# Performance work log

Measured on AMD Instinct MI355X. Metric: run time of the kernel, lower is better.

The kernel has to match this reference:

```python
import jax, jax.numpy as jnp
import numpy as np

EMB_DIM = 1024
NUM_HEADS = 16
HEAD_DIM = EMB_DIM // NUM_HEADS
B, S_Q, S_KV = 4, 2048, 2048


def setup_inputs() -> dict:
    key = jax.random.key(0)
    ks = jax.random.split(key, 12)
    s = EMB_DIM ** -0.5  # torch Linear default init scale (approx, uniform-like)
    inp = {
        "q": jax.random.normal(ks[0], (B, S_Q, EMB_DIM), jnp.float32),
        "k": jax.random.normal(ks[1], (B, S_KV, EMB_DIM), jnp.float32),
        "v": jax.random.normal(ks[2], (B, S_KV, EMB_DIM), jnp.float32),
        "mask": jax.random.randint(ks[3], (B, S_KV), 0, 2, jnp.int32),
        "Wq": jax.random.normal(ks[4], (EMB_DIM, EMB_DIM), jnp.float32) * s,
        "bq": jnp.zeros((EMB_DIM,), jnp.float32),
        "Wk": jax.random.normal(ks[5], (EMB_DIM, EMB_DIM), jnp.float32) * s,
        "bk": jnp.zeros((EMB_DIM,), jnp.float32),
        "Wv": jax.random.normal(ks[6], (EMB_DIM, EMB_DIM), jnp.float32) * s,
        "bv": jnp.zeros((EMB_DIM,), jnp.float32),
        "Wo": jax.random.normal(ks[7], (EMB_DIM, EMB_DIM), jnp.float32) * s,
        "bo": jnp.zeros((EMB_DIM,), jnp.float32),
    }
    return inp


def reference(q, k, v, mask, Wq, bq, Wk, bk, Wv, bv, Wo, bo):
    Bsz, Sq, E = q.shape
    Skv = k.shape[1]
    H, D = NUM_HEADS, HEAD_DIM
    scale = D ** -0.5

    # projections (torch Linear: x @ W.T + b)
    qh = (q @ Wq.T + bq).reshape(Bsz, Sq, H, D).transpose(0, 2, 1, 3)   # [B,H,Sq,D]
    kh = (k @ Wk.T + bk).reshape(Bsz, Skv, H, D).transpose(0, 2, 1, 3)  # [B,H,Skv,D]
    vh = (v @ Wv.T + bv).reshape(Bsz, Skv, H, D).transpose(0, 2, 1, 3)  # [B,H,Skv,D]

    attn = jnp.einsum("bhqd,bhkd->bhqk", qh, kh) * scale  # [B,H,Sq,Skv]

    valid = mask != 0                                      # [B,Skv]
    all_invalid = ~jnp.any(valid, axis=-1, keepdims=True)  # [B,1]
    safe = valid | all_invalid                             # reopened rows
    attn = jnp.where(safe[:, None, None, :], attn, -jnp.inf)

    attn = jax.nn.softmax(attn, axis=-1)
    attn = jnp.where(all_invalid.reshape(Bsz, 1, 1, 1), 0.0, attn)

    out = jnp.einsum("bhqk,bhkd->bhqd", attn, vh)          # [B,H,Sq,D]
    out = out.transpose(0, 2, 1, 3).reshape(Bsz, Sq, E)
    return out @ Wo.T + bo
```

## Files before the change

### kernel.cpp

```cpp
#include <hip/hip_runtime.h>
#include <hip/hip_bf16.h>

typedef short bh8 __attribute__((ext_vector_type(8)));
typedef float f32x4 __attribute__((ext_vector_type(4)));
typedef float f32x16 __attribute__((ext_vector_type(16)));
typedef float f2 __attribute__((ext_vector_type(2)));
typedef unsigned int uint4v __attribute__((ext_vector_type(4)));

#define GLOBAL_P(p) ((const __attribute__((address_space(1))) void*)(p))
#define LDS_P(p)    ((__attribute__((address_space(3))) void*)(p))

__device__ inline bh8 pack8(const float4& a, const float4& b) {
    union { bh8 v; __hip_bfloat16 h[8]; } u;
    u.h[0] = __float2bfloat16(a.x); u.h[1] = __float2bfloat16(a.y);
    u.h[2] = __float2bfloat16(a.z); u.h[3] = __float2bfloat16(a.w);
    u.h[4] = __float2bfloat16(b.x); u.h[5] = __float2bfloat16(b.y);
    u.h[6] = __float2bfloat16(b.z); u.h[7] = __float2bfloat16(b.w);
    return u.v;
}

__global__ __launch_bounds__(256) void cvt3(
    const float* __restrict__ a, const float* __restrict__ b, const float* __restrict__ c,
    __hip_bfloat16* __restrict__ oa, __hip_bfloat16* __restrict__ ob, __hip_bfloat16* __restrict__ oc)
{
    size_t i = ((size_t)blockIdx.x * 256 + threadIdx.x) * 8;
    float4 x0 = *(const float4*)(a + i), x1 = *(const float4*)(a + i + 4);
    *(bh8*)(oa + i) = pack8(x0, x1);
    float4 y0 = *(const float4*)(b + i), y1 = *(const float4*)(b + i + 4);
    *(bh8*)(ob + i) = pack8(y0, y1);
    float4 z0 = *(const float4*)(c + i), z1 = *(const float4*)(c + i + 4);
    *(bh8*)(oc + i) = pack8(z0, z1);
}

__global__ __launch_bounds__(256) void cvtW(
    const float* __restrict__ a, const float* __restrict__ b,
    const float* __restrict__ c, const float* __restrict__ d,
    __hip_bfloat16* __restrict__ o)
{
    int seg = blockIdx.x >> 9;
    const float* src = (seg == 0) ? a : (seg == 1) ? b : (seg == 2) ? c : d;
    size_t i = ((size_t)(blockIdx.x & 511) * 256 + threadIdx.x) * 8;
    float4 x0 = *(const float4*)(src + i), x1 = *(const float4*)(src + i + 4);
    *(bh8*)(o + (size_t)seg * 1048576 + i) = pack8(x0, x1);
}

template <typename TC>
__global__ __launch_bounds__(256) void gemm_bt(
    const __hip_bfloat16* __restrict__ A, const __hip_bfloat16* __restrict__ W,
    const float* __restrict__ bias, TC* __restrict__ C,
    int M, int N, int Ksz, float oscale)
{
    __shared__ __hip_bfloat16 As[128 * 64];
    __shared__ __hip_bfloat16 Bs[128 * 64];
    const int tid = threadIdx.x;
    const int l = tid & 63, w = tid >> 6;
    const int g4 = l >> 4, rl = l & 15;
    const int nb = N >> 7;
    const int bm = blockIdx.x / nb, bn = blockIdx.x % nb;
    const long m0 = (long)bm * 128, n0 = (long)bn * 128;

    const __hip_bfloat16* ag[4];
    const __hip_bfloat16* wg[4];
    int ldsbase[4];
#pragma unroll
    for (int i = 0; i < 4; ++i) {
        int c = i * 256 + tid;
        int row = c >> 3, c8 = c & 7;
        ag[i] = A + (m0 + row) * Ksz + c8 * 8;
        wg[i] = W + (n0 + row) * Ksz + c8 * 8;
        ldsbase[i] = (i * 256 + w * 64) * 8;
    }

    const int wr = w >> 1, wc = w & 1;
    f32x4 acc[4][4];
#pragma unroll
    for (int i = 0; i < 4; ++i)
#pragma unroll
        for (int j = 0; j < 4; ++j) acc[i][j] = f32x4{0.f, 0.f, 0.f, 0.f};

    const int nk = Ksz >> 6;
    for (int t = 0; t < nk; ++t) {
        __syncthreads();
#pragma unroll
        for (int i = 0; i < 4; ++i) {
            __builtin_amdgcn_global_load_lds(GLOBAL_P(ag[i]), LDS_P((__hip_bfloat16*)As + ldsbase[i]), 16, 0, 0);
            __builtin_amdgcn_global_load_lds(GLOBAL_P(wg[i]), LDS_P((__hip_bfloat16*)Bs + ldsbase[i]), 16, 0, 0);
            ag[i] += 64; wg[i] += 64;
        }
        __syncthreads();
#pragma unroll
        for (int kc = 0; kc < 2; ++kc) {
            bh8 af[4], bf[4];
#pragma unroll
            for (int mt = 0; mt < 4; ++mt) {
                int row = wr * 64 + mt * 16 + rl;
                af[mt] = *(const bh8*)(As + row * 64 + 8 * g4 + 32 * kc);
            }
#pragma unroll
            for (int nt = 0; nt < 4; ++nt) {
                int row = wc * 64 + nt * 16 + rl;
                bf[nt] = *(const bh8*)(Bs + row * 64 + 8 * g4 + 32 * kc);
            }
#pragma unroll
            for (int mt = 0; mt < 4; ++mt)
#pragma unroll
                for (int nt = 0; nt < 4; ++nt)
                    acc[mt][nt] = __builtin_amdgcn_mfma_f32_16x16x32_bf16(af[mt], bf[nt], acc[mt][nt], 0, 0, 0);
        }
    }

    float bv[4];
#pragma unroll
    for (int nt = 0; nt < 4; ++nt)
        bv[nt] = bias[n0 + wc * 64 + nt * 16 + rl];
#pragma unroll
    for (int mt = 0; mt < 4; ++mt) {
#pragma unroll
        for (int r = 0; r < 4; ++r) {
            long row = m0 + wr * 64 + mt * 16 + g4 * 4 + r;
            TC* cp = C + row * N + n0 + wc * 64 + rl;
#pragma unroll
            for (int nt = 0; nt < 4; ++nt) {
                float x = (acc[mt][nt][r] + bv[nt]) * oscale;
                if constexpr (__is_same(TC, float)) cp[nt * 16] = x;
                else cp[nt * 16] = __float2bfloat16(x);
            }
        }
    }
}

#define THRL 11.0f

__global__ __launch_bounds__(256, 2) void attn_kernel(
    const __hip_bfloat16* __restrict__ Qm, const __hip_bfloat16* __restrict__ Km,
    const __hip_bfloat16* __restrict__ Vm, const int* __restrict__ mask,
    __hip_bfloat16* __restrict__ Om)
{
    __shared__ __hip_bfloat16 Kt[2][64 * 64];
    __shared__ __hip_bfloat16 Vt[2][64 * 64];
    __shared__ float biasS[2048];
    const int tid = threadIdx.x;
    const int w = tid >> 6, l = tid & 63;
    const int G = l >> 5, c = l & 31;
    const int id = blockIdx.x;
    const int xcd = id & 7, slot = id >> 3;
    const int bh = xcd * 8 + (slot >> 4);
    const int qb = slot & 15;
    const int b = bh >> 4, h = bh & 15;
    const int q0 = qb * 128 + w * 32;

#pragma unroll
    for (int i = 0; i < 8; ++i) {
        int idx = i * 256 + tid;
        biasS[idx] = (mask[b * 2048 + idx] != 0) ? 0.f : -1e30f;
    }

    const __hip_bfloat16* qp = Qm + (size_t)(b * 2048 + q0 + c) * 1024 + h * 64 + 8 * G;
    bh8 qf[4];
#pragma unroll
    for (int kc = 0; kc < 4; ++kc) qf[kc] = *(const bh8*)(qp + 16 * kc);

    const int l38 = l >> 3, lc8 = l & 7;
    const __hip_bfloat16* kg0 = Km + (size_t)(b * 2048 + 16 * w + l38) * 1024 + h * 64 + 8 * ((lc8 ^ l38 ^ (2 * w)) & 7);
    const __hip_bfloat16* kg1 = Km + (size_t)(b * 2048 + 16 * w + 8 + l38) * 1024 + h * 64 + 8 * ((lc8 ^ l38 ^ (2 * w + 1)) & 7);
    const int kbase_e = w * 1024;

    const int vpi = tid >> 3, vd0 = (tid & 7) * 8;
    const __hip_bfloat16* vbase = Vm + (size_t)(b * 2048 + 2 * vpi) * 1024 + h * 64 + vd0;

    bh8 va0, va1;
    auto loadV = [&](int tt) {
        const __hip_bfloat16* vp = vbase + (size_t)tt * 64 * 1024;
        va0 = *(const bh8*)vp;
        va1 = *(const bh8*)(vp + 1024);
    };
    auto stageV = [&](int buf) {
        __hip_bfloat16* dst = &Vt[buf][0];
#pragma unroll
        for (int j = 0; j < 8; ++j) {
            int d = vd0 + j;
            int swz = ((d & 7) ^ (d >> 3)) << 3;
            unsigned lo = (unsigned short)((const short*)&va0)[j];
            unsigned hi = (unsigned short)((const short*)&va1)[j];
            *(unsigned*)&dst[(d * 64 + 2 * vpi) ^ swz] = lo | (hi << 16);
        }
    };
    auto stageK = [&](int buf, int tt) {
        const size_t off = (size_t)tt * 64 * 1024;
        __builtin_amdgcn_global_load_lds(GLOBAL_P(kg0 + off), LDS_P(&Kt[buf][0] + kbase_e), 16, 0, 0);
        __builtin_amdgcn_global_load_lds(GLOBAL_P(kg1 + off), LDS_P(&Kt[buf][0] + kbase_e + 512), 16, 0, 0);
    };

    stageK(0, 0);
    loadV(0);
    stageV(0);
    loadV(1);
    __syncthreads();

    f32x16 o0 = {0.f}, o1 = {0.f};
    float m_run = -1e29f, l_run = 0.f;

    for (int t = 0; t < 32; ++t) {
        const int buf = t & 1;
        if (t < 31) {
            stageK(buf ^ 1, t + 1);
            stageV(buf ^ 1);
            loadV(t + 2 < 32 ? t + 2 : 31);
        }
        __builtin_amdgcn_sched_barrier(0);

        const __hip_bfloat16* kbuf = &Kt[buf][0];
        const int kx0 = ((c & 7) ^ (c >> 3)) << 3;
        const int kx1 = kx0 ^ 32;
        f32x16 s0 = {0.f}, s1 = {0.f};
        __builtin_amdgcn_s_setprio(1);
#pragma unroll
        for (int kc = 0; kc < 4; ++kc) {
            bh8 kf = *(const bh8*)(kbuf + c * 64 + ((16 * kc + 8 * G) ^ kx0));
            s0 = __builtin_amdgcn_mfma_f32_32x32x16_bf16(kf, qf[kc], s0, 0, 0, 0);
        }
#pragma unroll
        for (int kc = 0; kc < 4; ++kc) {
            bh8 kf = *(const bh8*)(kbuf + (c + 32) * 64 + ((16 * kc + 8 * G) ^ kx1));
            s1 = __builtin_amdgcn_mfma_f32_32x32x16_bf16(kf, qf[kc], s1, 0, 0, 0);
        }
        __builtin_amdgcn_s_setprio(0);

        f2 mx2 = {-1e30f, -1e30f};
#pragma unroll
        for (int ct = 0; ct < 2; ++ct) {
            f2* sp = (f2*)(ct ? &s1 : &s0);
#pragma unroll
            for (int i2 = 0; i2 < 8; ++i2) {
                const int i = i2 * 2;
                f2 bb = *(const f2*)&biasS[t * 64 + ct * 32 + (i >> 2) * 8 + 4 * G + (i & 3)];
                f2 sv = sp[i2] + bb;
                sp[i2] = sv;
                mx2 = __builtin_elementwise_max(mx2, sv);
            }
        }
        float mxl = fmaxf(mx2[0], mx2[1]);

        if (__all(mxl - m_run <= THRL)) {
            f2 ls2 = {0.f, 0.f};
            f2 m2 = {m_run, m_run};
#pragma unroll
            for (int ct = 0; ct < 2; ++ct) {
                f2* sp = (f2*)(ct ? &s1 : &s0);
#pragma unroll
                for (int i2 = 0; i2 < 8; ++i2) {
                    f2 e = sp[i2] - m2;
                    f2 p;
                    p[0] = __builtin_amdgcn_exp2f(e[0]);
                    p[1] = __builtin_amdgcn_exp2f(e[1]);
                    sp[i2] = p; ls2 += p;
                }
            }
            l_run += ls2[0] + ls2[1];
        } else {
            float mxf = fmaxf(mxl, __shfl_xor(mxl, 32));
            const float m_new = fmaxf(m_run, mxf);
            const float fac = __builtin_amdgcn_exp2f(m_run - m_new);
            f2 ls2 = {0.f, 0.f};
            f2 m2 = {m_new, m_new};
#pragma unroll
            for (int ct = 0; ct < 2; ++ct) {
                f2* sp = (f2*)(ct ? &s1 : &s0);
#pragma unroll
                for (int i2 = 0; i2 < 8; ++i2) {
                    f2 e = sp[i2] - m2;
                    f2 p;
                    p[0] = __builtin_amdgcn_exp2f(e[0]);
                    p[1] = __builtin_amdgcn_exp2f(e[1]);
                    sp[i2] = p; ls2 += p;
                }
            }
            l_run = l_run * fac + (ls2[0] + ls2[1]);
            m_run = m_new;
            f2 fc = {fac, fac};
            f2* o0p = (f2*)&o0; f2* o1p = (f2*)&o1;
#pragma unroll
            for (int i2 = 0; i2 < 8; ++i2) { o0p[i2] *= fc; o1p[i2] *= fc; }
        }

        const __hip_bfloat16* vbuf = &Vt[buf][0];
        const int swz0 = ((c & 7) ^ (c >> 3)) << 3;
        const int swz1 = ((c & 7) ^ ((c + 32) >> 3)) << 3;
#pragma unroll
        for (int sl = 0; sl < 4; ++sl) {
            const f32x16& ps = (sl < 2) ? s0 : s1;
            const int R0 = 8 * (sl & 1);
            unsigned a0, a1, b0, b1;
            asm("v_cvt_pk_bf16_f32 %0, %1, %2" : "=v"(a0) : "v"(ps[R0 + 0]), "v"(ps[R0 + 1]));
            asm("v_cvt_pk_bf16_f32 %0, %1, %2" : "=v"(a1) : "v"(ps[R0 + 2]), "v"(ps[R0 + 3]));
            asm("v_cvt_pk_bf16_f32 %0, %1, %2" : "=v"(b0) : "v"(ps[R0 + 4]), "v"(ps[R0 + 5]));
            asm("v_cvt_pk_bf16_f32 %0, %1, %2" : "=v"(b1) : "v"(ps[R0 + 6]), "v"(ps[R0 + 7]));
            asm("v_permlane32_swap_b32 %0, %1" : "+v"(a0), "+v"(b0));
            asm("v_permlane32_swap_b32 %0, %1" : "+v"(a1), "+v"(b1));
            uint4v pu = {a0, a1, b0, b1};
            bh8 pf = __builtin_bit_cast(bh8, pu);
            const int kvb = 16 * sl + 8 * G;
            bh8 vf0 = *(const bh8*)(vbuf + c * 64 + (kvb ^ swz0));
            bh8 vf1 = *(const bh8*)(vbuf + (c + 32) * 64 + (kvb ^ swz1));
            __builtin_amdgcn_s_setprio(1);
            o0 = __builtin_amdgcn_mfma_f32_32x32x16_bf16(vf0, pf, o0, 0, 0, 0);
            o1 = __builtin_amdgcn_mfma_f32_32x32x16_bf16(vf1, pf, o1, 0, 0, 0);
            __builtin_amdgcn_s_setprio(0);
        }

        __syncthreads();
    }

    float l_tot = l_run + __shfl_xor(l_run, 32);
    float inv = (l_tot > 0.f) ? 1.f / l_tot : 0.f;
    __hip_bfloat16* op = Om + (size_t)(b * 2048 + q0 + c) * 1024 + h * 64 + 4 * G;
#pragma unroll
    for (int dt = 0; dt < 2; ++dt) {
#pragma unroll
        for (int rb = 0; rb < 4; ++rb) {
            union { ushort4 u; __hip_bfloat16 hv[4]; } cv;
#pragma unroll
            for (int j = 0; j < 4; ++j) {
                float x = (dt ? o1[rb * 4 + j] : o0[rb * 4 + j]) * inv;
                cv.hv[j] = __float2bfloat16(x);
            }
            *(ushort4*)(op + dt * 32 + rb * 8) = cv.u;
        }
    }
}

extern "C" void kernel_launch(void* const* d_in, const int* in_sizes, int n_in,
                              void* d_out, int out_size, void* d_ws, size_t ws_size,
                              hipStream_t stream) {
    const float* q  = (const float*)d_in[0];
    const float* k  = (const float*)d_in[1];
    const float* v  = (const float*)d_in[2];
    const int*   mk = (const int*)d_in[3];
    const float* Wq = (const float*)d_in[4];
    const float* bq = (const float*)d_in[5];
    const float* Wk = (const float*)d_in[6];
    const float* bk = (const float*)d_in[7];
    const float* Wv = (const float*)d_in[8];
    const float* bv = (const float*)d_in[9];
    const float* Wo = (const float*)d_in[10];
    const float* bo = (const float*)d_in[11];
    float* out = (float*)d_out;

    const float CSC = 0.18033688011112042f;
    const size_t MN = (size_t)8192 * 1024;
    const size_t WN = (size_t)1024 * 1024;
    __hip_bfloat16* B0 = (__hip_bfloat16*)d_ws;
    __hip_bfloat16* B1 = B0 + MN;
    __hip_bfloat16* B2 = B1 + MN;
    __hip_bfloat16* B3 = B2 + MN;
    __hip_bfloat16* Wb = B3 + MN;

    cvt3<<<4096, 256, 0, stream>>>(q, k, v, B0, B1, B2);
    cvtW<<<2048, 256, 0, stream>>>(Wq, Wk, Wv, Wo, Wb);
    gemm_bt<__hip_bfloat16><<<512, 256, 0, stream>>>(B0, Wb,          bq, B3, 8192, 1024, 1024, CSC);
    gemm_bt<__hip_bfloat16><<<512, 256, 0, stream>>>(B1, Wb + WN,     bk, B0, 8192, 1024, 1024, 1.0f);
    gemm_bt<__hip_bfloat16><<<512, 256, 0, stream>>>(B2, Wb + 2 * WN, bv, B1, 8192, 1024, 1024, 1.0f);
    attn_kernel<<<1024, 256, 0, stream>>>(B3, B0, B1, mk, B2);
    gemm_bt<float><<<512, 256, 0, stream>>>(B2, Wb + 3 * WN, bo, out, 8192, 1024, 1024, 1.0f);
}
```

Measured before the change: 253.1 us.

## Pre-transpose V in a separate kernel and stage it via direct global-to-LDS loads

Adds a transpose kernel that writes V per (batch, head) as a [64 x 2048] layout. The attention kernel can then load V tiles with the same async global_load_lds path used for K, instead of register loads followed by scattered LDS writes. This removes VALU and LDS-store work and register pressure from the main loop, and the occupancy hint is raised from 2 to 3 blocks per CU. The cost is an extra kernel launch plus a 16 MB read/write pass over V.

```diff
diff --git a/kernel.cpp b/kernel.cpp
--- a/kernel.cpp
+++ b/kernel.cpp
@@ -42,6 +42,39 @@
     size_t i = ((size_t)(blockIdx.x & 511) * 256 + threadIdx.x) * 8;
     float4 x0 = *(const float4*)(src + i), x1 = *(const float4*)(src + i + 4);
     *(bh8*)(o + (size_t)seg * 1048576 + i) = pack8(x0, x1);
+}
+
+__global__ __launch_bounds__(256) void transpV(
+    const __hip_bfloat16* __restrict__ Vw, __hip_bfloat16* __restrict__ Vt)
+{
+    __shared__ __hip_bfloat16 tile[64][66];
+    const int tid = threadIdx.x;
+    const int bh = blockIdx.x >> 5, kvb = blockIdx.x & 31;
+    const int b = bh >> 4, h = bh & 15;
+    {
+        const int r = tid >> 2, c0 = (tid & 3) * 16;
+        const __hip_bfloat16* src = Vw + (size_t)(b * 2048 + kvb * 64 + r) * 1024 + h * 64 + c0;
+        bh8 v0 = *(const bh8*)src;
+        bh8 v1 = *(const bh8*)(src + 8);
+#pragma unroll
+        for (int j = 0; j < 8; ++j) {
+            tile[r][c0 + j]     = ((const __hip_bfloat16*)&v0)[j];
+            tile[r][c0 + 8 + j] = ((const __hip_bfloat16*)&v1)[j];
+        }
+    }
+    __syncthreads();
+    {
+        const int d = tid >> 2, k0 = (tid & 3) * 16;
+        union { bh8 v; __hip_bfloat16 h8[8]; } o0, o1;
+#pragma unroll
+        for (int j = 0; j < 8; ++j) {
+            o0.h8[j] = tile[k0 + j][d];
+            o1.h8[j] = tile[k0 + 8 + j][d];
+        }
+        __hip_bfloat16* dst = Vt + ((size_t)bh * 64 + d) * 2048 + kvb * 64 + k0;
+        *(bh8*)dst = o0.v;
+        *(bh8*)(dst + 8) = o1.v;
+    }
 }
 
 template <typename TC>
@@ -131,9 +164,9 @@
 
 #define THRL 11.0f
 
-__global__ __launch_bounds__(256, 2) void attn_kernel(
+__global__ __launch_bounds__(256, 3) void attn_kernel(
     const __hip_bfloat16* __restrict__ Qm, const __hip_bfloat16* __restrict__ Km,
-    const __hip_bfloat16* __restrict__ Vm, const int* __restrict__ mask,
+    const __hip_bfloat16* __restrict__ Vt_g, const int* __restrict__ mask,
     __hip_bfloat16* __restrict__ Om)
 {
     __shared__ __hip_bfloat16 Kt[2][64 * 64];
@@ -163,38 +196,20 @@
     const int l38 = l >> 3, lc8 = l & 7;
     const __hip_bfloat16* kg0 = Km + (size_t)(b * 2048 + 16 * w + l38) * 1024 + h * 64 + 8 * ((lc8 ^ l38 ^ (2 * w)) & 7);
     const __hip_bfloat16* kg1 = Km + (size_t)(b * 2048 + 16 * w + 8 + l38) * 1024 + h * 64 + 8 * ((lc8 ^ l38 ^ (2 * w + 1)) & 7);
+    const __hip_bfloat16* vg0 = Vt_g + ((size_t)bh * 64 + 16 * w + l38) * 2048 + 8 * ((lc8 ^ l38 ^ (2 * w)) & 7);
+    const __hip_bfloat16* vg1 = Vt_g + ((size_t)bh * 64 + 16 * w + 8 + l38) * 2048 + 8 * ((lc8 ^ l38 ^ (2 * w + 1)) & 7);
     const int kbase_e = w * 1024;
 
-    const int vpi = tid >> 3, vd0 = (tid & 7) * 8;
-    const __hip_bfloat16* vbase = Vm + (size_t)(b * 2048 + 2 * vpi) * 1024 + h * 64 + vd0;
-
-    bh8 va0, va1;
-    auto loadV = [&](int tt) {
-        const __hip_bfloat16* vp = vbase + (size_t)tt * 64 * 1024;
-        va0 = *(const bh8*)vp;
-        va1 = *(const bh8*)(vp + 1024);
+    auto stageKV = [&](int buf, int tt) {
+        const size_t ko = (size_t)tt * 64 * 1024;
+        const size_t vo = (size_t)tt * 64;
+        __builtin_amdgcn_global_load_lds(GLOBAL_P(kg0 + ko), LDS_P(&Kt[buf][0] + kbase_e), 16, 0, 0);
+        __builtin_amdgcn_global_load_lds(GLOBAL_P(kg1 + ko), LDS_P(&Kt[buf][0] + kbase_e + 512), 16, 0, 0);
+        __builtin_amdgcn_global_load_lds(GLOBAL_P(vg0 + vo), LDS_P(&Vt[buf][0] + kbase_e), 16, 0, 0);
+        __builtin_amdgcn_global_load_lds(GLOBAL_P(vg1 + vo), LDS_P(&Vt[buf][0] + kbase_e + 512), 16, 0, 0);
     };
-    auto stageV = [&](int buf) {
-        __hip_bfloat16* dst = &Vt[buf][0];
-#pragma unroll
-        for (int j = 0; j < 8; ++j) {
-            int d = vd0 + j;
-            int swz = ((d & 7) ^ (d >> 3)) << 3;
-            unsigned lo = (unsigned short)((const short*)&va0)[j];
-            unsigned hi = (unsigned short)((const short*)&va1)[j];
-            *(unsigned*)&dst[(d * 64 + 2 * vpi) ^ swz] = lo | (hi << 16);
-        }
-    };
-    auto stageK = [&](int buf, int tt) {
-        const size_t off = (size_t)tt * 64 * 1024;
-        __builtin_amdgcn_global_load_lds(GLOBAL_P(kg0 + off), LDS_P(&Kt[buf][0] + kbase_e), 16, 0, 0);
-        __builtin_amdgcn_global_load_lds(GLOBAL_P(kg1 + off), LDS_P(&Kt[buf][0] + kbase_e + 512), 16, 0, 0);
-    };
-
-    stageK(0, 0);
-    loadV(0);
-    stageV(0);
-    loadV(1);
+
+    stageKV(0, 0);
     __syncthreads();
 
     f32x16 o0 = {0.f}, o1 = {0.f};
@@ -202,11 +217,7 @@
 
     for (int t = 0; t < 32; ++t) {
         const int buf = t & 1;
-        if (t < 31) {
-            stageK(buf ^ 1, t + 1);
-            stageV(buf ^ 1);
-            loadV(t + 2 < 32 ? t + 2 : 31);
-        }
+        if (t < 31) stageKV(buf ^ 1, t + 1);
         __builtin_amdgcn_sched_barrier(0);
 
         const __hip_bfloat16* kbuf = &Kt[buf][0];
@@ -284,8 +295,6 @@
         }
 
         const __hip_bfloat16* vbuf = &Vt[buf][0];
-        const int swz0 = ((c & 7) ^ (c >> 3)) << 3;
-        const int swz1 = ((c & 7) ^ ((c + 32) >> 3)) << 3;
 #pragma unroll
         for (int sl = 0; sl < 4; ++sl) {
             const f32x16& ps = (sl < 2) ? s0 : s1;
@@ -300,8 +309,8 @@
             uint4v pu = {a0, a1, b0, b1};
             bh8 pf = __builtin_bit_cast(bh8, pu);
             const int kvb = 16 * sl + 8 * G;
-            bh8 vf0 = *(const bh8*)(vbuf + c * 64 + (kvb ^ swz0));
-            bh8 vf1 = *(const bh8*)(vbuf + (c + 32) * 64 + (kvb ^ swz1));
+            bh8 vf0 = *(const bh8*)(vbuf + c * 64 + (kvb ^ kx0));
+            bh8 vf1 = *(const bh8*)(vbuf + (c + 32) * 64 + (kvb ^ kx1));
             __builtin_amdgcn_s_setprio(1);
             o0 = __builtin_amdgcn_mfma_f32_32x32x16_bf16(vf0, pf, o0, 0, 0, 0);
             o1 = __builtin_amdgcn_mfma_f32_32x32x16_bf16(vf1, pf, o1, 0, 0, 0);
@@ -354,12 +363,14 @@
     __hip_bfloat16* B2 = B1 + MN;
     __hip_bfloat16* B3 = B2 + MN;
     __hip_bfloat16* Wb = B3 + MN;
+    __hip_bfloat16* Vt = Wb + 4 * WN;
 
     cvt3<<<4096, 256, 0, stream>>>(q, k, v, B0, B1, B2);
     cvtW<<<2048, 256, 0, stream>>>(Wq, Wk, Wv, Wo, Wb);
     gemm_bt<__hip_bfloat16><<<512, 256, 0, stream>>>(B0, Wb,          bq, B3, 8192, 1024, 1024, CSC);
     gemm_bt<__hip_bfloat16><<<512, 256, 0, stream>>>(B1, Wb + WN,     bk, B0, 8192, 1024, 1024, 1.0f);
     gemm_bt<__hip_bfloat16><<<512, 256, 0, stream>>>(B2, Wb + 2 * WN, bv, B1, 8192, 1024, 1024, 1.0f);
-    attn_kernel<<<1024, 256, 0, stream>>>(B3, B0, B1, mk, B2);
+    transpV<<<2048, 256, 0, stream>>>(B1, Vt);
+    attn_kernel<<<1024, 256, 0, stream>>>(B3, B0, Vt, mk, B2);
     gemm_bt<float><<<512, 256, 0, stream>>>(B2, Wb + 3 * WN, bo, out, 8192, 1024, 1024, 1.0f);
 }
```

New measurement: 265.2 us. +4.8%, slower.

## Compact valid keys per batch and run attention only over unmasked tiles

Applied to the files above, without the earlier changes.

A new prefix-scan kernel builds, for each batch, a list of the indices of unmasked key positions and their count. A gather kernel copies the projected K and V rows into contiguous buffers, zero-padded to a multiple of 64. The attention kernel then loops only over the tiles that hold valid keys and derives its bias from the count instead of reading the mask, which skips the compute and loads for masked keys. In exchange it adds two kernel launches, an extra read and write of the valid K/V rows, and extra workspace. It also changes behaviour when every key in a batch is masked, since the loop then runs zero iterations.

```diff
diff --git a/kernel.cpp b/kernel.cpp
--- a/kernel.cpp
+++ b/kernel.cpp
@@ -42,6 +42,60 @@
     size_t i = ((size_t)(blockIdx.x & 511) * 256 + threadIdx.x) * 8;
     float4 x0 = *(const float4*)(src + i), x1 = *(const float4*)(src + i + 4);
     *(bh8*)(o + (size_t)seg * 1048576 + i) = pack8(x0, x1);
+}
+
+__global__ __launch_bounds__(256) void maskScan(
+    const int* __restrict__ mask, int* __restrict__ idx, int* __restrict__ nv)
+{
+    __shared__ int ts[256];
+    const int b = blockIdx.x, tid = threadIdx.x;
+    int f[8], cnt = 0;
+#pragma unroll
+    for (int j = 0; j < 8; ++j) {
+        f[j] = (mask[b * 2048 + tid * 8 + j] != 0) ? 1 : 0;
+        cnt += f[j];
+    }
+    ts[tid] = cnt;
+    __syncthreads();
+    for (int off = 1; off < 256; off <<= 1) {
+        int v = (tid >= off) ? ts[tid - off] : 0;
+        __syncthreads();
+        ts[tid] += v;
+        __syncthreads();
+    }
+    int base = ts[tid] - cnt;
+#pragma unroll
+    for (int j = 0; j < 8; ++j)
+        if (f[j]) idx[b * 2048 + base++] = tid * 8 + j;
+    if (tid == 255) nv[b] = ts[255];
+}
+
+__global__ __launch_bounds__(256) void gatherKV(
+    const __hip_bfloat16* __restrict__ Kw, const __hip_bfloat16* __restrict__ Vw,
+    const int* __restrict__ idx, const int* __restrict__ nv,
+    __hip_bfloat16* __restrict__ Kc, __hip_bfloat16* __restrict__ Vc)
+{
+    const int b = blockIdx.x >> 5, j = blockIdx.x & 31;
+    const int n = nv[b], npad = (n + 63) & ~63;
+    const int r = j * 64 + (threadIdx.x >> 2);
+    if (r >= npad) return;
+    const int c0 = (threadIdx.x & 3) * 256;
+    __hip_bfloat16* dk = Kc + ((size_t)b * 2048 + r) * 1024 + c0;
+    __hip_bfloat16* dv = Vc + ((size_t)b * 2048 + r) * 1024 + c0;
+    if (r < n) {
+        const int s = idx[b * 2048 + r];
+        const __hip_bfloat16* sk = Kw + ((size_t)b * 2048 + s) * 1024 + c0;
+        const __hip_bfloat16* sv = Vw + ((size_t)b * 2048 + s) * 1024 + c0;
+#pragma unroll
+        for (int i = 0; i < 32; ++i) {
+            ((bh8*)dk)[i] = ((const bh8*)sk)[i];
+            ((bh8*)dv)[i] = ((const bh8*)sv)[i];
+        }
+    } else {
+        bh8 z = {};
+#pragma unroll
+        for (int i = 0; i < 32; ++i) { ((bh8*)dk)[i] = z; ((bh8*)dv)[i] = z; }
+    }
 }
 
 template <typename TC>
@@ -133,7 +187,7 @@
 
 __global__ __launch_bounds__(256, 2) void attn_kernel(
     const __hip_bfloat16* __restrict__ Qm, const __hip_bfloat16* __restrict__ Km,
-    const __hip_bfloat16* __restrict__ Vm, const int* __restrict__ mask,
+    const __hip_bfloat16* __restrict__ Vm, const int* __restrict__ nvp,
     __hip_bfloat16* __restrict__ Om)
 {
     __shared__ __hip_bfloat16 Kt[2][64 * 64];
@@ -149,10 +203,13 @@
     const int b = bh >> 4, h = bh & 15;
     const int q0 = qb * 128 + w * 32;
 
+    const int n = nvp[b];
+    const int nt = (n + 63) >> 6;
+
 #pragma unroll
     for (int i = 0; i < 8; ++i) {
         int idx = i * 256 + tid;
-        biasS[idx] = (mask[b * 2048 + idx] != 0) ? 0.f : -1e30f;
+        biasS[idx] = (idx < n) ? 0.f : -1e30f;
     }
 
     const __hip_bfloat16* qp = Qm + (size_t)(b * 2048 + q0 + c) * 1024 + h * 64 + 8 * G;
@@ -194,18 +251,18 @@
     stageK(0, 0);
     loadV(0);
     stageV(0);
-    loadV(1);
+    loadV(nt > 1 ? 1 : 0);
     __syncthreads();
 
     f32x16 o0 = {0.f}, o1 = {0.f};
     float m_run = -1e29f, l_run = 0.f;
 
-    for (int t = 0; t < 32; ++t) {
+    for (int t = 0; t < nt; ++t) {
         const int buf = t & 1;
-        if (t < 31) {
+        if (t < nt - 1) {
             stageK(buf ^ 1, t + 1);
             stageV(buf ^ 1);
-            loadV(t + 2 < 32 ? t + 2 : 31);
+            loadV(t + 2 < nt ? t + 2 : nt - 1);
         }
         __builtin_amdgcn_sched_barrier(0);
 
@@ -349,17 +406,22 @@
     const float CSC = 0.18033688011112042f;
     const size_t MN = (size_t)8192 * 1024;
     const size_t WN = (size_t)1024 * 1024;
-    __hip_bfloat16* B0 = (__hip_bfloat16*)d_ws;
-    __hip_bfloat16* B1 = B0 + MN;
-    __hip_bfloat16* B2 = B1 + MN;
-    __hip_bfloat16* B3 = B2 + MN;
-    __hip_bfloat16* Wb = B3 + MN;
-
-    cvt3<<<4096, 256, 0, stream>>>(q, k, v, B0, B1, B2);
+    __hip_bfloat16* R0 = (__hip_bfloat16*)d_ws;
+    __hip_bfloat16* R1 = R0 + MN;
+    __hip_bfloat16* R2 = R1 + MN;
+    __hip_bfloat16* R3 = R2 + MN;
+    __hip_bfloat16* Wb = R3 + MN;
+    int* idxp = (int*)(Wb + 4 * WN);
+    int* nvp  = idxp + 4 * 2048;
+    __hip_bfloat16* Vc = (__hip_bfloat16*)((char*)idxp + 33024);
+
+    cvt3<<<4096, 256, 0, stream>>>(q, k, v, R0, R1, R2);
     cvtW<<<2048, 256, 0, stream>>>(Wq, Wk, Wv, Wo, Wb);
-    gemm_bt<__hip_bfloat16><<<512, 256, 0, stream>>>(B0, Wb,          bq, B3, 8192, 1024, 1024, CSC);
-    gemm_bt<__hip_bfloat16><<<512, 256, 0, stream>>>(B1, Wb + WN,     bk, B0, 8192, 1024, 1024, 1.0f);
-    gemm_bt<__hip_bfloat16><<<512, 256, 0, stream>>>(B2, Wb + 2 * WN, bv, B1, 8192, 1024, 1024, 1.0f);
-    attn_kernel<<<1024, 256, 0, stream>>>(B3, B0, B1, mk, B2);
-    gemm_bt<float><<<512, 256, 0, stream>>>(B2, Wb + 3 * WN, bo, out, 8192, 1024, 1024, 1.0f);
-}
+    maskScan<<<4, 256, 0, stream>>>(mk, idxp, nvp);
+    gemm_bt<__hip_bfloat16><<<512, 256, 0, stream>>>(R0, Wb,          bq, R3, 8192, 1024, 1024, CSC);
+    gemm_bt<__hip_bfloat16><<<512, 256, 0, stream>>>(R1, Wb + WN,     bk, R0, 8192, 1024, 1024, 1.0f);
+    gemm_bt<__hip_bfloat16><<<512, 256, 0, stream>>>(R2, Wb + 2 * WN, bv, R1, 8192, 1024, 1024, 1.0f);
+    gatherKV<<<128, 256, 0, stream>>>(R0, R1, idxp, nvp, R2, Vc);
+    attn_kernel<<<1024, 256, 0, stream>>>(R3, R2, Vc, nvp, R0);
+    gemm_bt<float><<<512, 256, 0, stream>>>(R0, Wb + 3 * WN, bo, out, 8192, 1024, 1024, 1.0f);
+}
```

Result: faster. 237.8 us (-6.0%).
